# Performance work log

Hardware: AMD Instinct MI355X
Metric: run time of the kernel (lower is better)

## Reference

```python
import jax, jax.numpy as jnp
import numpy as np

DIM = 20
N = 200000
E = 6400000
ITERATIONS = 3


def setup_inputs() -> dict:
    key = jax.random.key(0)
    ks = jax.random.split(key, 20)
    inp = {
        "h": jax.random.normal(ks[0], (N, DIM), dtype=jnp.float32),
        "node2depth": jax.random.randint(ks[1], (N,), 0, 5, dtype=jnp.int32),
        "edge_src": jax.random.randint(ks[2], (E,), 0, N, dtype=jnp.int32),
        "edge_dst": jax.random.randint(ks[3], (E,), 0, N, dtype=jnp.int32),
    }
    # Six DIM x DIM Linear layers (weight stored [out,in] like torch, plus bias)
    scale = 1.0 / np.sqrt(DIM)
    names = ["Wz", "Uz", "Wr", "Ur", "Wh", "Uh"]
    for j, nm in enumerate(names):
        inp[nm + "_w"] = jax.random.uniform(ks[4 + 2 * j], (DIM, DIM), jnp.float32, -scale, scale)
        inp[nm + "_b"] = jax.random.uniform(ks[5 + 2 * j], (DIM,), jnp.float32, -scale, scale)
    return inp


def _linear(x, w, b):
    return x @ w.T + b


def reference(h, Wz_w, Wz_b, Uz_w, Uz_b, Wr_w, Wr_b, Ur_w, Ur_b,
              Wh_w, Wh_b, Uh_w, Uh_b, node2depth, edge_src, edge_dst):
    active = None
    for i in range(ITERATIONS):
        # active set shrinks as i grows (depth + i <= ITERATIONS)
        active = (node2depth + i) <= ITERATIONS  # [N] bool
        af = active.astype(h.dtype)
        # x[u] = sum over neighbors v of h[v], counting only active src AND active dst
        msg = h[edge_src] * af[edge_src][:, None]          # [E, DIM]
        x = jax.ops.segment_sum(msg, edge_dst, num_segments=N)  # [N, DIM]
        x = x * af[:, None]
        z = jax.nn.sigmoid(_linear(x, Wz_w, Wz_b) + _linear(h, Uz_w, Uz_b))
        r = jax.nn.sigmoid(_linear(x, Wr_w, Wr_b) + _linear(h, Ur_w, Ur_b))
        h_cand = jnp.tanh(_linear(x, Wh_w, Wh_b) + _linear(r * h, Uh_w, Uh_b))
        h_new = z * h + (1.0 - z) * h_cand
        # inactive nodes are dropped from the dict in the original; since the
        # active set only shrinks, keeping their old h is equivalent
        h = jnp.where(active[:, None], h_new, h)
    # original returns only nodes active at the last iteration; zero out the rest
    return jnp.where(active[:, None], h, jnp.zeros_like(h))
```

## Files before the change

### kernel.cpp

```cpp
#include <hip/hip_runtime.h>

#define DIM    20
#define NN     200000
#define EE     6400000
#define ITERS  3
#define BLOCK  256

#define NODES_PER_FINE   64
#define NFINE            3125
#define NCOARSE          98
#define FINE_PER_COARSE  32
#define TILE             4096
#define IPT              16
#define XSTRIDE          21

typedef unsigned int u32;

__global__ __launch_bounds__(BLOCK) void k1_count(const int* __restrict__ edst,
                                                  int* __restrict__ fine_cnt) {
    __shared__ u32 lhist[NFINE];
    int tid = threadIdx.x;
    for (int i = tid; i < NFINE; i += BLOCK) lhist[i] = 0;
    __syncthreads();
    for (int e = blockIdx.x * BLOCK + tid; e < EE; e += gridDim.x * BLOCK) {
        int d = edst[e];
        atomicAdd(&lhist[d >> 6], 1u);
    }
    __syncthreads();
    for (int i = tid; i < NFINE; i += BLOCK) {
        u32 v = lhist[i];
        if (v) atomicAdd((u32*)&fine_cnt[i], v);
    }
}

__global__ __launch_bounds__(BLOCK) void k2_scan(const int* __restrict__ fine_cnt,
                                                 int* __restrict__ fine_base,
                                                 int* __restrict__ fine_cursor,
                                                 int* __restrict__ coarse_base,
                                                 int* __restrict__ coarse_cursor) {
    const int CH = 13;
    int tid = threadIdx.x;
    int loc[CH];
    int base = tid * CH;
    int s = 0;
    #pragma unroll
    for (int j = 0; j < CH; ++j) {
        int idx = base + j;
        int v = (idx < NFINE) ? fine_cnt[idx] : 0;
        loc[j] = v; s += v;
    }
    __shared__ int wsum[4];
    int lane = tid & 63, wid = tid >> 6;
    int incl = s;
    #pragma unroll
    for (int off = 1; off < 64; off <<= 1) {
        int t = __shfl_up(incl, off, 64);
        if (lane >= off) incl += t;
    }
    if (lane == 63) wsum[wid] = incl;
    __syncthreads();
    int woff = 0;
    for (int w = 0; w < wid; ++w) woff += wsum[w];
    int run = woff + incl - s;
    #pragma unroll
    for (int j = 0; j < CH; ++j) {
        int idx = base + j;
        if (idx < NFINE) {
            fine_base[idx]   = run;
            fine_cursor[idx] = run;
            run += loc[j];
        }
    }
    if (tid == 0) fine_base[NFINE] = EE;
    __syncthreads();
    if (tid < NCOARSE + 1) {
        int f = tid * FINE_PER_COARSE; if (f > NFINE) f = NFINE;
        int v = fine_base[f];
        coarse_base[tid] = v;
        if (tid < NCOARSE) coarse_cursor[tid] = v;
    }
}

__global__ __launch_bounds__(BLOCK) void p1_split(const int* __restrict__ esrc,
                                                  const int* __restrict__ edst,
                                                  const int* __restrict__ depth,
                                                  int* __restrict__ coarse_cursor,
                                                  u32* __restrict__ buf1) {
    __shared__ u32 lhist[NCOARSE];
    __shared__ u32 gbase[NCOARSE];
    int tid = threadIdx.x;
    int start = blockIdx.x * TILE;
    if (tid < NCOARSE) lhist[tid] = 0;
    __syncthreads();

    u32 item[IPT]; u32 key[IPT]; u32 rank[IPT];
    #pragma unroll
    for (int k = 0; k < IPT; ++k) {
        int e = start + k * BLOCK + tid;
        if (e < EE) {
            int d = edst[e];
            int s = esrc[e];
            u32 dep = (u32)depth[s];
            u32 c = (u32)d >> 11;
            key[k]  = c;
            item[k] = ((u32)d & 2047u) | ((u32)s << 11) | (dep << 29);
            rank[k] = atomicAdd(&lhist[c], 1u);
        }
    }
    __syncthreads();
    if (tid < NCOARSE) {
        u32 cnt = lhist[tid];
        gbase[tid] = cnt ? (u32)atomicAdd((u32*)&coarse_cursor[tid], cnt) : 0u;
    }
    __syncthreads();
    #pragma unroll
    for (int k = 0; k < IPT; ++k) {
        int e = start + k * BLOCK + tid;
        if (e < EE) buf1[gbase[key[k]] + rank[k]] = item[k];
    }
}

__global__ __launch_bounds__(BLOCK) void p2_split(const u32* __restrict__ buf1,
                                                  const int* __restrict__ coarse_base,
                                                  int* __restrict__ fine_cursor,
                                                  u32* __restrict__ buf2) {
    __shared__ u32 lhist[2 * FINE_PER_COARSE];
    __shared__ u32 gbase[2 * FINE_PER_COARSE];
    __shared__ int cb[NCOARSE + 1];
    __shared__ int sc0;
    int tid = threadIdx.x;
    int start = blockIdx.x * TILE;
    if (tid < NCOARSE + 1) cb[tid] = coarse_base[tid];
    if (tid < 2 * FINE_PER_COARSE) { lhist[tid] = 0; gbase[tid] = 0; }
    __syncthreads();
    if (tid == 0) {
        int c = 0;
        while (c + 1 < NCOARSE && cb[c + 1] <= start) ++c;
        sc0 = c;
    }
    __syncthreads();
    int c0 = sc0;
    int b1 = cb[c0 + 1];

    u32 item[IPT]; u32 key[IPT]; u32 rank[IPT];
    #pragma unroll
    for (int k = 0; k < IPT; ++k) {
        int i = start + k * BLOCK + tid;
        if (i < EE) {
            u32 w = buf1[i];
            u32 dlow = w & 2047u;
            u32 sdep = w >> 11;
            u32 kk = ((i < b1) ? 0u : (u32)FINE_PER_COARSE) + (dlow >> 6);
            key[k]  = kk;
            item[k] = (dlow & 63u) | (sdep << 6);
            rank[k] = atomicAdd(&lhist[kk], 1u);
        }
    }
    __syncthreads();
    if (tid < 2 * FINE_PER_COARSE) {
        u32 cnt = lhist[tid];
        int idx = c0 * FINE_PER_COARSE + tid;
        if (cnt && idx < NFINE)
            gbase[tid] = (u32)atomicAdd((u32*)&fine_cursor[idx], cnt);
    }
    __syncthreads();
    #pragma unroll
    for (int k = 0; k < IPT; ++k) {
        int i = start + k * BLOCK + tid;
        if (i < EE) buf2[gbase[key[k]] + rank[k]] = item[k];
    }
}

__global__ __launch_bounds__(BLOCK) void pb_sort(const u32* __restrict__ buf2,
                                                 const int* __restrict__ fine_base,
                                                 int* __restrict__ ptr,
                                                 u32* __restrict__ cnt3,
                                                 u32* __restrict__ ssrc) {
    __shared__ u32 hist[512];
    __shared__ u32 ebase[512];
    __shared__ u32 lout[TILE];
    __shared__ u32 wsum[4];
    int tid = threadIdx.x;
    int b = blockIdx.x;
    int lo = fine_base[b];
    int hi = fine_base[b + 1];
    int cnt = hi - lo;
    hist[tid] = 0; hist[tid + 256] = 0;
    __syncthreads();

    u32 item[IPT]; u32 key[IPT]; u32 rank[IPT];
    #pragma unroll
    for (int k = 0; k < IPT; ++k) {
        int i = lo + k * BLOCK + tid;
        if (i < hi) {
            u32 w = buf2[i];
            u32 kk = (w & 63u) * 8u + (w >> 24);
            key[k]  = kk;
            item[k] = (w >> 6) & 0x3FFFFu;
            rank[k] = atomicAdd(&hist[kk], 1u);
        }
    }
    __syncthreads();
    {
        u32 s0 = hist[2 * tid], s1 = hist[2 * tid + 1];
        u32 s = s0 + s1;
        int lane = tid & 63, wid = tid >> 6;
        u32 incl = s;
        #pragma unroll
        for (int off = 1; off < 64; off <<= 1) {
            u32 t = __shfl_up((int)incl, off, 64);
            if (lane >= off) incl += t;
        }
        if (lane == 63) wsum[wid] = incl;
        __syncthreads();
        u32 woff = 0;
        for (int w = 0; w < wid; ++w) woff += wsum[w];
        u32 excl = woff + incl - s;
        ebase[2 * tid]     = excl;
        ebase[2 * tid + 1] = excl + s0;
    }
    __syncthreads();
    if (tid < NODES_PER_FINE) {
        u32 base0 = ebase[tid * 8];
        u32 c1 = ebase[tid * 8 + 2] - base0;
        u32 c2 = ebase[tid * 8 + 3] - base0;
        u32 c3 = ebase[tid * 8 + 4] - base0;
        int u = b * NODES_PER_FINE + tid;
        ptr[u]  = lo + (int)base0;
        cnt3[u] = c1 | (c2 << 10) | (c3 << 20);
    }
    #pragma unroll
    for (int k = 0; k < IPT; ++k) {
        int i = lo + k * BLOCK + tid;
        if (i < hi) lout[ebase[key[k]] + rank[k]] = item[k];
    }
    __syncthreads();
    for (int j = tid; j < cnt; j += BLOCK) ssrc[lo + j] = lout[j];
}

__device__ __forceinline__ u32 pack_bf16x2(float a, float b) {
    u32 ua = __float_as_uint(a);
    u32 ub = __float_as_uint(b);
    ua = (ua + 0x7FFFu + ((ua >> 16) & 1u)) >> 16;
    ub = (ub + 0x7FFFu + ((ub >> 16) & 1u)) & 0xFFFF0000u;
    return ua | ub;
}

__global__ __launch_bounds__(BLOCK) void hconv(const float* __restrict__ h,
                                               u32* __restrict__ hb) {
    int g = blockIdx.x * BLOCK + threadIdx.x;
    if (g >= NN * 16) return;
    int node = g >> 4, slot = g & 15;
    u32 v = 0;
    if (slot < 10) {
        float2 f = *(const float2*)(h + (size_t)node * DIM + slot * 2);
        v = pack_bf16x2(f.x, f.y);
    }
    hb[g] = v;
}


__device__ __forceinline__ float bl(u32 w) { return __uint_as_float(w << 16); }
__device__ __forceinline__ float bh(u32 w) { return __uint_as_float(w & 0xFFFF0000u); }

__device__ __forceinline__ void acc_bf16row(float* x, uint4 A, uint4 B, uint2 C) {
    x[0]+=bl(A.x);  x[1]+=bh(A.x);  x[2]+=bl(A.y);  x[3]+=bh(A.y);
    x[4]+=bl(A.z);  x[5]+=bh(A.z);  x[6]+=bl(A.w);  x[7]+=bh(A.w);
    x[8]+=bl(B.x);  x[9]+=bh(B.x);  x[10]+=bl(B.y); x[11]+=bh(B.y);
    x[12]+=bl(B.z); x[13]+=bh(B.z); x[14]+=bl(B.w); x[15]+=bh(B.w);
    x[16]+=bl(C.x); x[17]+=bh(C.x); x[18]+=bl(C.y); x[19]+=bh(C.y);
}

__device__ __forceinline__ float fast_sigmoid(float t) {
    return 1.0f / (1.0f + __expf(-t));
}
__device__ __forceinline__ float fast_tanh(float t) {
    t = fminf(fmaxf(t, -15.0f), 15.0f);
    float e2 = __expf(2.0f * t);
    return (e2 - 1.0f) / (e2 + 1.0f);
}

__global__ __launch_bounds__(BLOCK) void grnn_iter(
    const float* __restrict__ h_in, float* __restrict__ h_out,
    const u32* __restrict__ hb_in, u32* __restrict__ hb_out,
    const int* __restrict__ depth, const int* __restrict__ ptr,
    const u32* __restrict__ cnt3, const u32* __restrict__ ssrc,
    const float* __restrict__ Wz, const float* __restrict__ bWz,
    const float* __restrict__ Uz, const float* __restrict__ bUz,
    const float* __restrict__ Wr, const float* __restrict__ bWr,
    const float* __restrict__ Ur, const float* __restrict__ bUr,
    const float* __restrict__ Wh, const float* __restrict__ bWh,
    const float* __restrict__ Uh, const float* __restrict__ bUh,
    int it, int shift, int isFinal)
{
    __shared__ float xl[64 * XSTRIDE];
    int tid = threadIdx.x;
    int nl  = tid >> 2;
    int t   = tid & 3;
    int lim = ITERS - it;

    {
        int u = blockIdx.x * 64 + nl;
        if (depth[u] <= lim) {
            int p = ptr[u];
            int d = (int)((cnt3[u] >> shift) & 1023u);
            float x[DIM];
            #pragma unroll
            for (int k = 0; k < DIM; ++k) x[k] = 0.0f;
            int e = t;
            for (; e + 4 < d; e += 8) {
                u32 v0 = ssrc[p + e];
                u32 v1 = ssrc[p + e + 4];
                const u32* r0 = hb_in + (size_t)v0 * 16;
                const u32* r1 = hb_in + (size_t)v1 * 16;
                uint4 A0 = *(const uint4*)r0; uint4 B0 = *(const uint4*)(r0 + 4);
                uint2 C0 = *(const uint2*)(r0 + 8);
                uint4 A1 = *(const uint4*)r1; uint4 B1 = *(const uint4*)(r1 + 4);
                uint2 C1 = *(const uint2*)(r1 + 8);
                acc_bf16row(x, A0, B0, C0);
                acc_bf16row(x, A1, B1, C1);
            }
            if (e < d) {
                u32 v0 = ssrc[p + e];
                const u32* r0 = hb_in + (size_t)v0 * 16;
                uint4 A0 = *(const uint4*)r0; uint4 B0 = *(const uint4*)(r0 + 4);
                uint2 C0 = *(const uint2*)(r0 + 8);
                acc_bf16row(x, A0, B0, C0);
            }
            #pragma unroll
            for (int k = 0; k < DIM; ++k) {
                x[k] += __shfl_xor(x[k], 1, 64);
                x[k] += __shfl_xor(x[k], 2, 64);
            }
            float* xr = xl + nl * XSTRIDE;
            #pragma unroll
            for (int q = 0; q < 5; ++q) xr[q * 4 + t] = x[q * 4 + t];
        }
    }
    __syncthreads();
    if (tid >= 64) return;

    int u = blockIdx.x * 64 + tid;
    bool act = depth[u] <= lim;
    if (!act) {
        if (isFinal) {
            float4 z4 = make_float4(0.f, 0.f, 0.f, 0.f);
            float4* o4 = (float4*)(h_out + (size_t)u * DIM);
            #pragma unroll
            for (int q = 0; q < 5; ++q) o4[q] = z4;
        }
        return;
    }

    float x[DIM], h[DIM];
    #pragma unroll
    for (int k = 0; k < DIM; ++k) x[k] = xl[tid * XSTRIDE + k];
    {
        const float4* hv = (const float4*)(h_in + (size_t)u * DIM);
        float4 a0 = hv[0], a1 = hv[1], a2 = hv[2], a3 = hv[3], a4 = hv[4];
        h[0]=a0.x; h[1]=a0.y; h[2]=a0.z; h[3]=a0.w;
        h[4]=a1.x; h[5]=a1.y; h[6]=a1.z; h[7]=a1.w;
        h[8]=a2.x; h[9]=a2.y; h[10]=a2.z; h[11]=a2.w;
        h[12]=a3.x; h[13]=a3.y; h[14]=a3.z; h[15]=a3.w;
        h[16]=a4.x; h[17]=a4.y; h[18]=a4.z; h[19]=a4.w;
    }

    float z[DIM], rh[DIM];
    #pragma unroll
    for (int j = 0; j < DIM; ++j) {
        float sz = bWz[j] + bUz[j];
        float sr = bWr[j] + bUr[j];
        #pragma unroll
        for (int k = 0; k < DIM; ++k) {
            sz += x[k] * Wz[j * DIM + k];
            sz += h[k] * Uz[j * DIM + k];
            sr += x[k] * Wr[j * DIM + k];
            sr += h[k] * Ur[j * DIM + k];
        }
        z[j]  = fast_sigmoid(sz);
        rh[j] = fast_sigmoid(sr) * h[j];
    }

    float o[DIM];
    #pragma unroll
    for (int j = 0; j < DIM; ++j) {
        float sh = bWh[j] + bUh[j];
        #pragma unroll
        for (int k = 0; k < DIM; ++k) {
            sh += x[k]  * Wh[j * DIM + k];
            sh += rh[k] * Uh[j * DIM + k];
        }
        float hc = fast_tanh(sh);
        o[j] = z[j] * h[j] + (1.0f - z[j]) * hc;
    }

    {
        float4* o4 = (float4*)(h_out + (size_t)u * DIM);
        o4[0] = make_float4(o[0],  o[1],  o[2],  o[3]);
        o4[1] = make_float4(o[4],  o[5],  o[6],  o[7]);
        o4[2] = make_float4(o[8],  o[9],  o[10], o[11]);
        o4[3] = make_float4(o[12], o[13], o[14], o[15]);
        o4[4] = make_float4(o[16], o[17], o[18], o[19]);
    }
    if (!isFinal) {
        u32* row = hb_out + (size_t)u * 16;
        uint4 wA = make_uint4(pack_bf16x2(o[0], o[1]),  pack_bf16x2(o[2], o[3]),
                              pack_bf16x2(o[4], o[5]),  pack_bf16x2(o[6], o[7]));
        uint4 wB = make_uint4(pack_bf16x2(o[8], o[9]),  pack_bf16x2(o[10], o[11]),
                              pack_bf16x2(o[12], o[13]), pack_bf16x2(o[14], o[15]));
        uint2 wC = make_uint2(pack_bf16x2(o[16], o[17]), pack_bf16x2(o[18], o[19]));
        *(uint4*)row       = wA;
        *(uint4*)(row + 4) = wB;
        *(uint2*)(row + 8) = wC;
    }
}


extern "C" void kernel_launch(void* const* d_in, const int* in_sizes, int n_in,
                              void* d_out, int out_size, void* d_ws, size_t ws_size,
                              hipStream_t stream) {
    const float* h0    = (const float*)d_in[0];
    const int*   depth = (const int*)d_in[1];
    const int*   esrc  = (const int*)d_in[2];
    const int*   edst  = (const int*)d_in[3];
    const float* Wz  = (const float*)d_in[4];  const float* bWz = (const float*)d_in[5];
    const float* Uz  = (const float*)d_in[6];  const float* bUz = (const float*)d_in[7];
    const float* Wr  = (const float*)d_in[8];  const float* bWr = (const float*)d_in[9];
    const float* Ur  = (const float*)d_in[10]; const float* bUr = (const float*)d_in[11];
    const float* Wh  = (const float*)d_in[12]; const float* bWh = (const float*)d_in[13];
    const float* Uh  = (const float*)d_in[14]; const float* bUh = (const float*)d_in[15];
    float* out = (float*)d_out;

    int* W = (int*)d_ws;
    int*  fine_cnt      = W + 0;
    int*  fine_base     = W + 3200;
    int*  fine_cursor   = W + 6400;
    int*  coarse_base   = W + 9600;
    int*  coarse_cursor = W + 9728;
    int*  ptr           = W + 9856;
    u32*  cnt3          = (u32*)(W + 209920);
    u32*  buf1          = (u32*)(W + 409984);
    u32*  buf2          = buf1 + EE;
    float* h1           = (float*)(buf2 + EE);
    u32*  hbA           = (u32*)(h1 + (size_t)NN * DIM);
    u32*  hbB           = hbA + (size_t)NN * 16;
    u32*  ssrc          = buf1;
    float* h2           = (float*)buf2;

    hipMemsetAsync(fine_cnt, 0, NFINE * sizeof(int), stream);

    int ntile = (EE + TILE - 1) / TILE;

    k1_count<<<256, BLOCK, 0, stream>>>(edst, fine_cnt);
    k2_scan <<<1,   BLOCK, 0, stream>>>(fine_cnt, fine_base, fine_cursor,
                                        coarse_base, coarse_cursor);
    p1_split<<<ntile, BLOCK, 0, stream>>>(esrc, edst, depth, coarse_cursor, buf1);
    p2_split<<<ntile, BLOCK, 0, stream>>>(buf1, coarse_base, fine_cursor, buf2);
    pb_sort <<<NFINE, BLOCK, 0, stream>>>(buf2, fine_base, ptr, cnt3, ssrc);
    hconv   <<<(NN * 16) / BLOCK, BLOCK, 0, stream>>>(h0, hbA);

    grnn_iter<<<NFINE, BLOCK, 0, stream>>>(h0, h1, hbA, hbB, depth, ptr, cnt3, ssrc,
        Wz, bWz, Uz, bUz, Wr, bWr, Ur, bUr, Wh, bWh, Uh, bUh, 0, 20, 0);
    grnn_iter<<<NFINE, BLOCK, 0, stream>>>(h1, h2, hbB, hbA, depth, ptr, cnt3, ssrc,
        Wz, bWz, Uz, bUz, Wr, bWr, Ur, bUr, Wh, bWh, Uh, bUh, 1, 10, 0);
    grnn_iter<<<NFINE, BLOCK, 0, stream>>>(h2, out, hbA, hbB, depth, ptr, cnt3, ssrc,
        Wz, bWz, Uz, bUz, Wr, bWr, Ur, bUr, Wh, bWh, Uh, bUh, 2, 0, 1);
}
```

Baseline: 519.2 us.

## Renumber nodes by depth and split gather from GRU update

Adds a depth-sorted permutation of nodes so the bf16 hidden-state table is laid out with shallow (longer-active) nodes first. Edge source ids are stored as permuted ids, and only still-needed rows are written back, which shrinks the gathered working set. The fused per-iteration kernel is split into a gather kernel (8 lanes per node) and a separate GRU update kernel, and the double-buffered bf16 table becomes a single buffer. This trades extra launches and a round trip of x through global memory for better cache locality on the random gathers.

Result: slower. 541.1 us (+4.2%).

```diff
diff --git a/kernel.cpp b/kernel.cpp
--- a/kernel.cpp
+++ b/kernel.cpp
@@ -12,78 +12,136 @@
 #define FINE_PER_COARSE  32
 #define TILE             4096
 #define IPT              16
-#define XSTRIDE          21
 
 typedef unsigned int u32;
 
 __global__ __launch_bounds__(BLOCK) void k1_count(const int* __restrict__ edst,
-                                                  int* __restrict__ fine_cnt) {
+                                                  const int* __restrict__ depth,
+                                                  int* __restrict__ fine_cnt,
+                                                  int* __restrict__ dcnt) {
     __shared__ u32 lhist[NFINE];
+    __shared__ u32 dh[5];
     int tid = threadIdx.x;
     for (int i = tid; i < NFINE; i += BLOCK) lhist[i] = 0;
+    if (tid < 5) dh[tid] = 0;
     __syncthreads();
     for (int e = blockIdx.x * BLOCK + tid; e < EE; e += gridDim.x * BLOCK) {
         int d = edst[e];
         atomicAdd(&lhist[d >> 6], 1u);
     }
+    for (int n = blockIdx.x * BLOCK + tid; n < NN; n += gridDim.x * BLOCK) {
+        atomicAdd(&dh[depth[n]], 1u);
+    }
     __syncthreads();
     for (int i = tid; i < NFINE; i += BLOCK) {
         u32 v = lhist[i];
         if (v) atomicAdd((u32*)&fine_cnt[i], v);
     }
+    if (tid < 5) dcnt[tid * 256 + blockIdx.x] = (int)dh[tid];
 }
 
 __global__ __launch_bounds__(BLOCK) void k2_scan(const int* __restrict__ fine_cnt,
                                                  int* __restrict__ fine_base,
                                                  int* __restrict__ fine_cursor,
                                                  int* __restrict__ coarse_base,
-                                                 int* __restrict__ coarse_cursor) {
-    const int CH = 13;
-    int tid = threadIdx.x;
-    int loc[CH];
-    int base = tid * CH;
-    int s = 0;
-    #pragma unroll
-    for (int j = 0; j < CH; ++j) {
-        int idx = base + j;
-        int v = (idx < NFINE) ? fine_cnt[idx] : 0;
-        loc[j] = v; s += v;
-    }
+                                                 int* __restrict__ coarse_cursor,
+                                                 const int* __restrict__ dcnt,
+                                                 int* __restrict__ dbase,
+                                                 int* __restrict__ cum) {
     __shared__ int wsum[4];
+    __shared__ int sdb[1281];
+    int tid = threadIdx.x;
     int lane = tid & 63, wid = tid >> 6;
-    int incl = s;
-    #pragma unroll
-    for (int off = 1; off < 64; off <<= 1) {
-        int t = __shfl_up(incl, off, 64);
-        if (lane >= off) incl += t;
-    }
-    if (lane == 63) wsum[wid] = incl;
-    __syncthreads();
-    int woff = 0;
-    for (int w = 0; w < wid; ++w) woff += wsum[w];
-    int run = woff + incl - s;
-    #pragma unroll
-    for (int j = 0; j < CH; ++j) {
-        int idx = base + j;
-        if (idx < NFINE) {
-            fine_base[idx]   = run;
-            fine_cursor[idx] = run;
+
+    {
+        const int CH = 13;
+        int loc[CH];
+        int base = tid * CH;
+        int s = 0;
+        #pragma unroll
+        for (int j = 0; j < CH; ++j) {
+            int idx = base + j;
+            int v = (idx < NFINE) ? fine_cnt[idx] : 0;
+            loc[j] = v; s += v;
+        }
+        int incl = s;
+        #pragma unroll
+        for (int off = 1; off < 64; off <<= 1) {
+            int t = __shfl_up(incl, off, 64);
+            if (lane >= off) incl += t;
+        }
+        if (lane == 63) wsum[wid] = incl;
+        __syncthreads();
+        int woff = 0;
+        for (int w = 0; w < wid; ++w) woff += wsum[w];
+        int run = woff + incl - s;
+        #pragma unroll
+        for (int j = 0; j < CH; ++j) {
+            int idx = base + j;
+            if (idx < NFINE) {
+                fine_base[idx]   = run;
+                fine_cursor[idx] = run;
+                run += loc[j];
+            }
+        }
+        if (tid == 0) fine_base[NFINE] = EE;
+        __syncthreads();
+        if (tid < NCOARSE + 1) {
+            int f = tid * FINE_PER_COARSE; if (f > NFINE) f = NFINE;
+            int v = fine_base[f];
+            coarse_base[tid] = v;
+            if (tid < NCOARSE) coarse_cursor[tid] = v;
+        }
+    }
+    __syncthreads();
+
+    {
+        const int CH2 = 5;
+        int loc[CH2];
+        int base = tid * CH2;
+        int s = 0;
+        #pragma unroll
+        for (int j = 0; j < CH2; ++j) { int v = dcnt[base + j]; loc[j] = v; s += v; }
+        int incl = s;
+        #pragma unroll
+        for (int off = 1; off < 64; off <<= 1) {
+            int t = __shfl_up(incl, off, 64);
+            if (lane >= off) incl += t;
+        }
+        if (lane == 63) wsum[wid] = incl;
+        __syncthreads();
+        int woff = 0;
+        for (int w = 0; w < wid; ++w) woff += wsum[w];
+        int run = woff + incl - s;
+        #pragma unroll
+        for (int j = 0; j < CH2; ++j) {
+            sdb[base + j]   = run;
+            dbase[base + j] = run;
             run += loc[j];
         }
-    }
-    if (tid == 0) fine_base[NFINE] = EE;
-    __syncthreads();
-    if (tid < NCOARSE + 1) {
-        int f = tid * FINE_PER_COARSE; if (f > NFINE) f = NFINE;
-        int v = fine_base[f];
-        coarse_base[tid] = v;
-        if (tid < NCOARSE) coarse_cursor[tid] = v;
+        if (tid == 255) sdb[1280] = run;
+        __syncthreads();
+        if (tid < 5) cum[tid] = sdb[(tid + 1) * 256];
+    }
+}
+
+__global__ __launch_bounds__(BLOCK) void kd_scatter(const int* __restrict__ depth,
+                                                    const int* __restrict__ dbase,
+                                                    int* __restrict__ perm) {
+    __shared__ u32 dh[5];
+    int tid = threadIdx.x;
+    if (tid < 5) dh[tid] = 0;
+    __syncthreads();
+    for (int n = blockIdx.x * BLOCK + tid; n < NN; n += gridDim.x * BLOCK) {
+        int d = depth[n];
+        u32 r = atomicAdd(&dh[d], 1u);
+        perm[n] = dbase[d * 256 + blockIdx.x] + (int)r;
     }
 }
 
 __global__ __launch_bounds__(BLOCK) void p1_split(const int* __restrict__ esrc,
                                                   const int* __restrict__ edst,
-                                                  const int* __restrict__ depth,
+                                                  const int* __restrict__ perm,
                                                   int* __restrict__ coarse_cursor,
                                                   u32* __restrict__ buf1) {
     __shared__ u32 lhist[NCOARSE];
@@ -100,10 +158,10 @@
         if (e < EE) {
             int d = edst[e];
             int s = esrc[e];
-            u32 dep = (u32)depth[s];
+            u32 pid = (u32)perm[s];
             u32 c = (u32)d >> 11;
             key[k]  = c;
-            item[k] = ((u32)d & 2047u) | ((u32)s << 11) | (dep << 29);
+            item[k] = ((u32)d & 2047u) | (pid << 11);
             rank[k] = atomicAdd(&lhist[c], 1u);
         }
     }
@@ -149,10 +207,10 @@
         if (i < EE) {
             u32 w = buf1[i];
             u32 dlow = w & 2047u;
-            u32 sdep = w >> 11;
+            u32 pid  = w >> 11;
             u32 kk = ((i < b1) ? 0u : (u32)FINE_PER_COARSE) + (dlow >> 6);
             key[k]  = kk;
-            item[k] = (dlow & 63u) | (sdep << 6);
+            item[k] = (dlow & 63u) | (pid << 6);
             rank[k] = atomicAdd(&lhist[kk], 1u);
         }
     }
@@ -173,6 +231,7 @@
 
 __global__ __launch_bounds__(BLOCK) void pb_sort(const u32* __restrict__ buf2,
                                                  const int* __restrict__ fine_base,
+                                                 const int* __restrict__ cum,
                                                  int* __restrict__ ptr,
                                                  u32* __restrict__ cnt3,
                                                  u32* __restrict__ ssrc) {
@@ -185,6 +244,7 @@
     int lo = fine_base[b];
     int hi = fine_base[b + 1];
     int cnt = hi - lo;
+    u32 c0 = (u32)cum[0], c1 = (u32)cum[1], c2 = (u32)cum[2], c3 = (u32)cum[3];
     hist[tid] = 0; hist[tid + 256] = 0;
     __syncthreads();
 
@@ -194,9 +254,12 @@
         int i = lo + k * BLOCK + tid;
         if (i < hi) {
             u32 w = buf2[i];
-            u32 kk = (w & 63u) * 8u + (w >> 24);
+            u32 pid = w >> 6;
+            u32 dep = (u32)(pid >= c0) + (u32)(pid >= c1)
+                    + (u32)(pid >= c2) + (u32)(pid >= c3);
+            u32 kk = (w & 63u) * 8u + dep;
             key[k]  = kk;
-            item[k] = (w >> 6) & 0x3FFFFu;
+            item[k] = pid;
             rank[k] = atomicAdd(&hist[kk], 1u);
         }
     }
@@ -222,12 +285,12 @@
     __syncthreads();
     if (tid < NODES_PER_FINE) {
         u32 base0 = ebase[tid * 8];
-        u32 c1 = ebase[tid * 8 + 2] - base0;
-        u32 c2 = ebase[tid * 8 + 3] - base0;
-        u32 c3 = ebase[tid * 8 + 4] - base0;
+        u32 cc1 = ebase[tid * 8 + 2] - base0;
+        u32 cc2 = ebase[tid * 8 + 3] - base0;
+        u32 cc3 = ebase[tid * 8 + 4] - base0;
         int u = b * NODES_PER_FINE + tid;
         ptr[u]  = lo + (int)base0;
-        cnt3[u] = c1 | (c2 << 10) | (c3 << 20);
+        cnt3[u] = cc1 | (cc2 << 10) | (cc3 << 20);
     }
     #pragma unroll
     for (int k = 0; k < IPT; ++k) {
@@ -247,16 +310,16 @@
 }
 
 __global__ __launch_bounds__(BLOCK) void hconv(const float* __restrict__ h,
-                                               u32* __restrict__ hb) {
+                                               u32* __restrict__ hb,
+                                               const int* __restrict__ perm,
+                                               const int* __restrict__ depth) {
     int g = blockIdx.x * BLOCK + threadIdx.x;
     if (g >= NN * 16) return;
     int node = g >> 4, slot = g & 15;
-    u32 v = 0;
-    if (slot < 10) {
-        float2 f = *(const float2*)(h + (size_t)node * DIM + slot * 2);
-        v = pack_bf16x2(f.x, f.y);
-    }
-    hb[g] = v;
+    if (slot >= 10) return;
+    if (depth[node] > ITERS) return;
+    float2 f = *(const float2*)(h + (size_t)node * DIM + slot * 2);
+    hb[(size_t)perm[node] * 16 + slot] = pack_bf16x2(f.x, f.y);
 }
 
 
@@ -271,6 +334,55 @@
     x[16]+=bl(C.x); x[17]+=bh(C.x); x[18]+=bl(C.y); x[19]+=bh(C.y);
 }
 
+__global__ __launch_bounds__(BLOCK) void gather_x(
+    const u32* __restrict__ hb,
+    const int* __restrict__ depth, const int* __restrict__ ptr,
+    const u32* __restrict__ cnt3, const u32* __restrict__ ssrc,
+    float* __restrict__ xg, int lim, int shift)
+{
+    int tid = threadIdx.x;
+    int u = blockIdx.x * 32 + (tid >> 3);
+    int t = tid & 7;
+    if (depth[u] > lim) return;
+    int p = ptr[u];
+    int d = (int)((cnt3[u] >> shift) & 1023u);
+    float x[DIM];
+    #pragma unroll
+    for (int k = 0; k < DIM; ++k) x[k] = 0.0f;
+
+    int e = t;
+    for (; e + 8 < d; e += 16) {
+        u32 v0 = ssrc[p + e];
+        u32 v1 = ssrc[p + e + 8];
+        const u32* r0 = hb + (size_t)v0 * 16;
+        const u32* r1 = hb + (size_t)v1 * 16;
+        uint4 A0 = *(const uint4*)r0; uint4 B0 = *(const uint4*)(r0 + 4);
+        uint2 C0 = *(const uint2*)(r0 + 8);
+        uint4 A1 = *(const uint4*)r1; uint4 B1 = *(const uint4*)(r1 + 4);
+        uint2 C1 = *(const uint2*)(r1 + 8);
+        acc_bf16row(x, A0, B0, C0);
+        acc_bf16row(x, A1, B1, C1);
+    }
+    if (e < d) {
+        u32 v0 = ssrc[p + e];
+        const u32* r0 = hb + (size_t)v0 * 16;
+        uint4 A0 = *(const uint4*)r0; uint4 B0 = *(const uint4*)(r0 + 4);
+        uint2 C0 = *(const uint2*)(r0 + 8);
+        acc_bf16row(x, A0, B0, C0);
+    }
+    #pragma unroll
+    for (int k = 0; k < DIM; ++k) {
+        x[k] += __shfl_xor(x[k], 1, 64);
+        x[k] += __shfl_xor(x[k], 2, 64);
+        x[k] += __shfl_xor(x[k], 4, 64);
+    }
+    float* xr = xg + (size_t)u * DIM;
+    xr[t]     = x[t];
+    xr[t + 8] = x[t + 8];
+    if (t < 4) xr[t + 16] = x[t + 16];
+}
+
+
 __device__ __forceinline__ float fast_sigmoid(float t) {
     return 1.0f / (1.0f + __expf(-t));
 }
@@ -280,67 +392,22 @@
     return (e2 - 1.0f) / (e2 + 1.0f);
 }
 
-__global__ __launch_bounds__(BLOCK) void grnn_iter(
+__global__ __launch_bounds__(BLOCK) void gru_update(
+    const float* __restrict__ xg,
     const float* __restrict__ h_in, float* __restrict__ h_out,
-    const u32* __restrict__ hb_in, u32* __restrict__ hb_out,
-    const int* __restrict__ depth, const int* __restrict__ ptr,
-    const u32* __restrict__ cnt3, const u32* __restrict__ ssrc,
+    u32* __restrict__ hb_out,
+    const int* __restrict__ depth, const int* __restrict__ perm,
+    const int* __restrict__ cum,
     const float* __restrict__ Wz, const float* __restrict__ bWz,
     const float* __restrict__ Uz, const float* __restrict__ bUz,
     const float* __restrict__ Wr, const float* __restrict__ bWr,
     const float* __restrict__ Ur, const float* __restrict__ bUr,
     const float* __restrict__ Wh, const float* __restrict__ bWh,
     const float* __restrict__ Uh, const float* __restrict__ bUh,
-    int it, int shift, int isFinal)
+    int lim, int cumIdx, int isFinal)
 {
-    __shared__ float xl[64 * XSTRIDE];
-    int tid = threadIdx.x;
-    int nl  = tid >> 2;
-    int t   = tid & 3;
-    int lim = ITERS - it;
-
-    {
-        int u = blockIdx.x * 64 + nl;
-        if (depth[u] <= lim) {
-            int p = ptr[u];
-            int d = (int)((cnt3[u] >> shift) & 1023u);
-            float x[DIM];
-            #pragma unroll
-            for (int k = 0; k < DIM; ++k) x[k] = 0.0f;
-            int e = t;
-            for (; e + 4 < d; e += 8) {
-                u32 v0 = ssrc[p + e];
-                u32 v1 = ssrc[p + e + 4];
-                const u32* r0 = hb_in + (size_t)v0 * 16;
-                const u32* r1 = hb_in + (size_t)v1 * 16;
-                uint4 A0 = *(const uint4*)r0; uint4 B0 = *(const uint4*)(r0 + 4);
-                uint2 C0 = *(const uint2*)(r0 + 8);
-                uint4 A1 = *(const uint4*)r1; uint4 B1 = *(const uint4*)(r1 + 4);
-                uint2 C1 = *(const uint2*)(r1 + 8);
-                acc_bf16row(x, A0, B0, C0);
-                acc_bf16row(x, A1, B1, C1);
-            }
-            if (e < d) {
-                u32 v0 = ssrc[p + e];
-                const u32* r0 = hb_in + (size_t)v0 * 16;
-                uint4 A0 = *(const uint4*)r0; uint4 B0 = *(const uint4*)(r0 + 4);
-                uint2 C0 = *(const uint2*)(r0 + 8);
-                acc_bf16row(x, A0, B0, C0);
-            }
-            #pragma unroll
-            for (int k = 0; k < DIM; ++k) {
-                x[k] += __shfl_xor(x[k], 1, 64);
-                x[k] += __shfl_xor(x[k], 2, 64);
-            }
-            float* xr = xl + nl * XSTRIDE;
-            #pragma unroll
-            for (int q = 0; q < 5; ++q) xr[q * 4 + t] = x[q * 4 + t];
-        }
-    }
-    __syncthreads();
-    if (tid >= 64) return;
-
-    int u = blockIdx.x * 64 + tid;
+    int u = blockIdx.x * BLOCK + threadIdx.x;
+    if (u >= NN) return;
     bool act = depth[u] <= lim;
     if (!act) {
         if (isFinal) {
@@ -353,8 +420,15 @@
     }
 
     float x[DIM], h[DIM];
-    #pragma unroll
-    for (int k = 0; k < DIM; ++k) x[k] = xl[tid * XSTRIDE + k];
+    {
+        const float4* xv = (const float4*)(xg + (size_t)u * DIM);
+        float4 a0 = xv[0], a1 = xv[1], a2 = xv[2], a3 = xv[3], a4 = xv[4];
+        x[0]=a0.x; x[1]=a0.y; x[2]=a0.z; x[3]=a0.w;
+        x[4]=a1.x; x[5]=a1.y; x[6]=a1.z; x[7]=a1.w;
+        x[8]=a2.x; x[9]=a2.y; x[10]=a2.z; x[11]=a2.w;
+        x[12]=a3.x; x[13]=a3.y; x[14]=a3.z; x[15]=a3.w;
+        x[16]=a4.x; x[17]=a4.y; x[18]=a4.z; x[19]=a4.w;
+    }
     {
         const float4* hv = (const float4*)(h_in + (size_t)u * DIM);
         float4 a0 = hv[0], a1 = hv[1], a2 = hv[2], a3 = hv[3], a4 = hv[4];
@@ -403,15 +477,18 @@
         o4[4] = make_float4(o[16], o[17], o[18], o[19]);
     }
     if (!isFinal) {
-        u32* row = hb_out + (size_t)u * 16;
-        uint4 wA = make_uint4(pack_bf16x2(o[0], o[1]),  pack_bf16x2(o[2], o[3]),
-                              pack_bf16x2(o[4], o[5]),  pack_bf16x2(o[6], o[7]));
-        uint4 wB = make_uint4(pack_bf16x2(o[8], o[9]),  pack_bf16x2(o[10], o[11]),
-                              pack_bf16x2(o[12], o[13]), pack_bf16x2(o[14], o[15]));
-        uint2 wC = make_uint2(pack_bf16x2(o[16], o[17]), pack_bf16x2(o[18], o[19]));
-        *(uint4*)row       = wA;
-        *(uint4*)(row + 4) = wB;
-        *(uint2*)(row + 8) = wC;
+        int pid = perm[u];
+        if (pid < cum[cumIdx]) {
+            u32* row = hb_out + (size_t)pid * 16;
+            uint4 wA = make_uint4(pack_bf16x2(o[0], o[1]),  pack_bf16x2(o[2], o[3]),
+                                  pack_bf16x2(o[4], o[5]),  pack_bf16x2(o[6], o[7]));
+            uint4 wB = make_uint4(pack_bf16x2(o[8], o[9]),  pack_bf16x2(o[10], o[11]),
+                                  pack_bf16x2(o[12], o[13]), pack_bf16x2(o[14], o[15]));
+            uint2 wC = make_uint2(pack_bf16x2(o[16], o[17]), pack_bf16x2(o[18], o[19]));
+            *(uint4*)row       = wA;
+            *(uint4*)(row + 4) = wB;
+            *(uint2*)(row + 8) = wC;
+        }
     }
 }
 
@@ -437,32 +514,39 @@
     int*  fine_cursor   = W + 6400;
     int*  coarse_base   = W + 9600;
     int*  coarse_cursor = W + 9728;
-    int*  ptr           = W + 9856;
-    u32*  cnt3          = (u32*)(W + 209920);
-    u32*  buf1          = (u32*)(W + 409984);
+    int*  dcnt          = W + 9856;
+    int*  dbase         = W + 11200;
+    int*  cum           = W + 12544;
+    int*  ptr           = W + 12800;
+    u32*  cnt3          = (u32*)(W + 212864);
+    int*  perm          = W + 412864;
+    u32*  buf1          = (u32*)(W + 612864);
     u32*  buf2          = buf1 + EE;
     float* h1           = (float*)(buf2 + EE);
-    u32*  hbA           = (u32*)(h1 + (size_t)NN * DIM);
-    u32*  hbB           = hbA + (size_t)NN * 16;
+    u32*  hb            = (u32*)(h1 + (size_t)NN * DIM);
     u32*  ssrc          = buf1;
-    float* h2           = (float*)buf2;
+    float* xg           = (float*)buf2;
 
     hipMemsetAsync(fine_cnt, 0, NFINE * sizeof(int), stream);
 
     int ntile = (EE + TILE - 1) / TILE;
 
-    k1_count<<<256, BLOCK, 0, stream>>>(edst, fine_cnt);
-    k2_scan <<<1,   BLOCK, 0, stream>>>(fine_cnt, fine_base, fine_cursor,
-                                        coarse_base, coarse_cursor);
-    p1_split<<<ntile, BLOCK, 0, stream>>>(esrc, edst, depth, coarse_cursor, buf1);
-    p2_split<<<ntile, BLOCK, 0, stream>>>(buf1, coarse_base, fine_cursor, buf2);
-    pb_sort <<<NFINE, BLOCK, 0, stream>>>(buf2, fine_base, ptr, cnt3, ssrc);
-    hconv   <<<(NN * 16) / BLOCK, BLOCK, 0, stream>>>(h0, hbA);
-
-    grnn_iter<<<NFINE, BLOCK, 0, stream>>>(h0, h1, hbA, hbB, depth, ptr, cnt3, ssrc,
-        Wz, bWz, Uz, bUz, Wr, bWr, Ur, bUr, Wh, bWh, Uh, bUh, 0, 20, 0);
-    grnn_iter<<<NFINE, BLOCK, 0, stream>>>(h1, h2, hbB, hbA, depth, ptr, cnt3, ssrc,
-        Wz, bWz, Uz, bUz, Wr, bWr, Ur, bUr, Wh, bWh, Uh, bUh, 1, 10, 0);
-    grnn_iter<<<NFINE, BLOCK, 0, stream>>>(h2, out, hbA, hbB, depth, ptr, cnt3, ssrc,
-        Wz, bWz, Uz, bUz, Wr, bWr, Ur, bUr, Wh, bWh, Uh, bUh, 2, 0, 1);
-}
+    k1_count  <<<256, BLOCK, 0, stream>>>(edst, depth, fine_cnt, dcnt);
+    k2_scan   <<<1,   BLOCK, 0, stream>>>(fine_cnt, fine_base, fine_cursor,
+                                          coarse_base, coarse_cursor, dcnt, dbase, cum);
+    kd_scatter<<<256, BLOCK, 0, stream>>>(depth, dbase, perm);
+    p1_split  <<<ntile, BLOCK, 0, stream>>>(esrc, edst, perm, coarse_cursor, buf1);
+    p2_split  <<<ntile, BLOCK, 0, stream>>>(buf1, coarse_base, fine_cursor, buf2);
+    pb_sort   <<<NFINE, BLOCK, 0, stream>>>(buf2, fine_base, cum, ptr, cnt3, ssrc);
+    hconv     <<<(NN * 16) / BLOCK, BLOCK, 0, stream>>>(h0, hb, perm, depth);
+
+    gather_x  <<<NN / 32, BLOCK, 0, stream>>>(hb, depth, ptr, cnt3, ssrc, xg, 3, 20);
+    gru_update<<<(NN + BLOCK - 1) / BLOCK, BLOCK, 0, stream>>>(xg, h0, h1, hb, depth, perm, cum,
+        Wz, bWz, Uz, bUz, Wr, bWr, Ur, bUr, Wh, bWh, Uh, bUh, 3, 2, 0);
+    gather_x  <<<NN / 32, BLOCK, 0, stream>>>(hb, depth, ptr, cnt3, ssrc, xg, 2, 10);
+    gru_update<<<(NN + BLOCK - 1) / BLOCK, BLOCK, 0, stream>>>(xg, h1, h1, hb, depth, perm, cum,
+        Wz, bWz, Uz, bUz, Wr, bWr, Ur, bUr, Wh, bWh, Uh, bUh, 2, 1, 0);
+    gather_x  <<<NN / 32, BLOCK, 0, stream>>>(hb, depth, ptr, cnt3, ssrc, xg, 1, 0);
+    gru_update<<<(NN + BLOCK - 1) / BLOCK, BLOCK, 0, stream>>>(xg, h1, out, hb, depth, perm, cum,
+        Wz, bWz, Uz, bUz, Wr, bWr, Ur, bUr, Wh, bWh, Uh, bUh, 1, 0, 1);
+}
```
